# Kernel tuning notes

Hardware: AMD Instinct MI355X
Metric: run time of the kernel (lower is better)

Reference implementation:

```python
import jax, jax.numpy as jnp
import numpy as np

OUTCOMES = [8, 8, 8, 8, 8, 8]           # concept outcome counts (concepts_order)
N_TOTAL = int(np.prod(OUTCOMES))        # 262144 joint states
N_VALID = 8192                          # admissible states
B, D = 4096, 1024


def setup_inputs() -> dict:
    key = jax.random.key(0)
    k1, k2 = jax.random.split(key)
    embeddings = jax.random.normal(k1, (B, D), dtype=jnp.float32)
    W = jax.random.normal(k2, (N_VALID, D), dtype=jnp.float32) * 0.02
    b = jnp.zeros((N_VALID,), dtype=jnp.float32)
    # unique sorted admissible-state indices, like torch.argwhere(mask)
    rng = np.random.default_rng(0)
    valid_states = jnp.asarray(
        np.sort(rng.choice(N_TOTAL, size=N_VALID, replace=False)).astype(np.int32))
    return {"embeddings": embeddings, "W": W, "b": b, "valid_states": valid_states}


def reference(embeddings, W, b, valid_states):
    # softmax over valid states: [B, N_VALID]
    probs = jax.nn.softmax(embeddings @ W.T + b, axis=1)
    probs_t = probs.T  # [N_VALID, B] for leading-axis segment reduction
    marginals = []
    stride = N_TOTAL
    for n_i in OUTCOMES:
        stride //= n_i
        # digit of each valid joint-state index along this concept's axis
        digit = (valid_states // stride) % n_i  # [N_VALID]
        # equivalent to scattering probs into the full joint tensor and
        # summing over all other concept axes, without materializing it
        m = jax.ops.segment_sum(probs_t, digit, num_segments=n_i).T  # [B, n_i]
        marginals.append(m)
    return jnp.stack(marginals)  # [n_concepts, B, 8]
```

## Files before the change

kernel.cpp:

```cpp
#include <hip/hip_runtime.h>
#include <hip/hip_bf16.h>
#include <cstdint>
#include <cstddef>

typedef __bf16 bf16_t;
typedef bf16_t bf16x8 __attribute__((ext_vector_type(8)));
typedef bf16_t bf16x4 __attribute__((ext_vector_type(4)));
typedef float  f32x4  __attribute__((ext_vector_type(4)));
typedef unsigned int u32;

#define BROWS 4096
#define NV    8192
#define KD    1024
#define NT    16
#define ST    48
#define LOG2E 1.44269504088896340736f

#define GLL(gsrc, ldst) \
  __builtin_amdgcn_global_load_lds((const __attribute__((address_space(1))) u32*)(gsrc), \
                                   (__attribute__((address_space(3))) u32*)(ldst), 16, 0, 0)
#define FENCE asm volatile("" ::: "memory")

__global__ void cvt_kernel(const float* __restrict__ src, bf16_t* __restrict__ dst, int n4) {
  int idx = blockIdx.x * blockDim.x + threadIdx.x;
  int stride = gridDim.x * blockDim.x;
  for (int i = idx; i < n4; i += stride) {
    float4 v = ((const float4*)src)[i];
    bf16x4 o;
    o[0] = (bf16_t)v.x; o[1] = (bf16_t)v.y; o[2] = (bf16_t)v.z; o[3] = (bf16_t)v.w;
    ((bf16x4*)dst)[i] = o;
  }
}

__global__ void build_s2t_kernel(const int* __restrict__ vstate, bf16_t* __restrict__ s2t) {
  int g = blockIdx.x * blockDim.x + threadIdx.x;
  if (g >= ST * NV) return;
  int b = g >> 13;
  int ig = g & (NV - 1);
  int c = b >> 3;
  int d = b & 7;
  int src = ig ^ ((b & 7) << 3);
  int dig = (vstate[src] >> (15 - 3 * c)) & 7;
  s2t[g] = (bf16_t)(dig == d ? 1.0f : 0.0f);
}

__global__ __launch_bounds__(512, 2)
void gemm_fused_kernel(const bf16_t* __restrict__ W, const bf16_t* __restrict__ E,
                       const float* __restrict__ bias, const bf16_t* __restrict__ s2t,
                       float* __restrict__ part) {
  __shared__ __align__(16) char lds[2][65536];
  #define AKH0 0
  #define AKH1 16384
  #define BKH0 32768
  #define BKH1 49152

  const int t    = threadIdx.x;
  const int lane = t & 63;
  const int wv   = t >> 6;
  const int wm   = wv >> 2;
  const int wn   = wv & 3;
  const int fr   = lane & 15;
  const int fq   = lane >> 4;

  int bid = blockIdx.x;
  int wg  = (bid & 7) * 64 + (bid >> 3);
  const int stile = wg >> 4;
  const int btile = wg & 15;
  const int st0 = stile * 256;
  const int bt0 = btile * 256;

  const int srow = lane >> 2;
  const int skel = ((lane & 3) ^ ((lane >> 3) & 3)) * 8;
  const bf16_t* aptr = W + (size_t)(st0 + wv * 32 + srow) * KD + skel;
  const bf16_t* bptr = E + (size_t)(bt0 + wv * 32 + srow) * KD + skel;
  const int dchunk = (wv * 2) * 1024;

  const int xsw = (fr & 6) << 3;
  const int base_a = (((wm * 128 + fr) * 64 + fq * 16) ^ xsw);
  const int base_b = 32768 + (((wn * 64 + fr) * 64 + fq * 16) ^ xsw);

  f32x4 acc[8][4] = {};

  GLL(aptr, &lds[0][AKH0 + dchunk]);
  GLL(aptr + 16 * KD, &lds[0][AKH0 + dchunk + 1024]);
  GLL(bptr, &lds[0][BKH0 + dchunk]);
  GLL(bptr + 16 * KD, &lds[0][BKH0 + dchunk + 1024]);
  GLL(aptr + 32, &lds[0][AKH1 + dchunk]);
  GLL(aptr + 32 + 16 * KD, &lds[0][AKH1 + dchunk + 1024]);
  GLL(bptr + 32, &lds[0][BKH1 + dchunk]);
  GLL(bptr + 32 + 16 * KD, &lds[0][BKH1 + dchunk + 1024]);
  asm volatile("s_waitcnt vmcnt(0)" ::: "memory");
  __builtin_amdgcn_s_barrier();
  FENCE;

  int cur = 0;
  for (int kt = 0; kt < NT; ++kt) {
    const char* bufp = lds[cur];
    char* nbuf = lds[cur ^ 1];
    const bool pf = (kt + 1 < NT);

    bf16x8 a0[8], b0[4], a1[8], b1[4];

#pragma unroll
    for (int n = 0; n < 4; ++n)
      b0[n] = *(const bf16x8*)(bufp + base_b + n * 1024);
#pragma unroll
    for (int m = 0; m < 8; ++m)
      a0[m] = *(const bf16x8*)(bufp + base_a + m * 1024);

    if (pf) {
      const bf16_t* an = aptr + (kt + 1) * 64;
      const bf16_t* bn = bptr + (kt + 1) * 64;
      GLL(an, &nbuf[AKH0 + dchunk]);
      GLL(an + 16 * KD, &nbuf[AKH0 + dchunk + 1024]);
      GLL(bn, &nbuf[BKH0 + dchunk]);
      GLL(bn + 16 * KD, &nbuf[BKH0 + dchunk + 1024]);
      GLL(an + 32, &nbuf[AKH1 + dchunk]);
      GLL(an + 32 + 16 * KD, &nbuf[AKH1 + dchunk + 1024]);
      GLL(bn + 32, &nbuf[BKH1 + dchunk]);
      GLL(bn + 32 + 16 * KD, &nbuf[BKH1 + dchunk + 1024]);
    }

#pragma unroll
    for (int n = 0; n < 4; ++n)
      b1[n] = *(const bf16x8*)(bufp + base_b + 16384 + n * 1024);
#pragma unroll
    for (int m = 0; m < 8; ++m)
      a1[m] = *(const bf16x8*)(bufp + base_a + 16384 + m * 1024);

    __builtin_amdgcn_s_setprio(1);
#pragma unroll
    for (int m = 0; m < 8; ++m)
#pragma unroll
      for (int n = 0; n < 4; ++n)
        acc[m][n] = __builtin_amdgcn_mfma_f32_16x16x32_bf16(a0[m], b0[n], acc[m][n], 0, 0, 0);
#pragma unroll
    for (int m = 0; m < 8; ++m)
#pragma unroll
      for (int n = 0; n < 4; ++n)
        acc[m][n] = __builtin_amdgcn_mfma_f32_16x16x32_bf16(a1[m], b1[n], acc[m][n], 0, 0, 0);
    __builtin_amdgcn_s_setprio(0);

    asm volatile("s_waitcnt vmcnt(0)" ::: "memory");
    __builtin_amdgcn_sched_barrier(0);
    __builtin_amdgcn_s_barrier();
    FENCE;
    cur ^= 1;
  }

  char* const ldsf = &lds[0][0];
  {
#pragma unroll
    for (int q = 0; q < 3; ++q) {
      const bf16_t* src = s2t + (size_t)(wv * 6 + q * 2 + (lane >> 5)) * NV
                          + st0 + (lane & 31) * 8;
      GLL(src, ldsf + 65536 + wv * 3072 + q * 1024);
    }
  }

  float* const ppart = part + ((size_t)stile * BROWS + bt0) * ST;

#pragma unroll
  for (int pass = 0; pass < 2; ++pass) {
    if ((wn >> 1) == pass) {
#pragma unroll
      for (int m = 0; m < 8; ++m) {
        const float4 bb = *(const float4*)&bias[st0 + wm * 128 + m * 16 + fq * 4];
#pragma unroll
        for (int n = 0; n < 4; ++n) {
          bf16x4 ev;
          ev[0] = (bf16_t)exp2f((acc[m][n][0] + bb.x) * LOG2E);
          ev[1] = (bf16_t)exp2f((acc[m][n][1] + bb.y) * LOG2E);
          ev[2] = (bf16_t)exp2f((acc[m][n][2] + bb.z) * LOG2E);
          ev[3] = (bf16_t)exp2f((acc[m][n][3] + bb.w) * LOG2E);
          const int jh = (wn & 1) * 64 + n * 16 + fr;
          const int ib = (wm * 128 + m * 16 + fq * 4) * 2;
          *(bf16x4*)(ldsf + jh * 512 + (ib ^ ((fr & 7) << 4))) = ev;
        }
      }
    }
    if (pass == 0) asm volatile("s_waitcnt vmcnt(0)" ::: "memory");
    __syncthreads();

    f32x4 acc2[3] = {{0.f,0.f,0.f,0.f},{0.f,0.f,0.f,0.f},{0.f,0.f,0.f,0.f}};
#pragma unroll
    for (int k2 = 0; k2 < 8; ++k2) {
      const int ko = (k2 * 64 + fq * 16) ^ ((fr & 7) << 4);
      const bf16x8 ea = *(const bf16x8*)(ldsf + (wv * 16 + fr) * 512 + ko);
#pragma unroll
      for (int n2 = 0; n2 < 3; ++n2) {
        const bf16x8 sb = *(const bf16x8*)(ldsf + 65536 + (n2 * 16 + fr) * 512 + ko);
        acc2[n2] = __builtin_amdgcn_mfma_f32_16x16x32_bf16(ea, sb, acc2[n2], 0, 0, 0);
      }
    }
    const int jg = pass * 128 + wv * 16 + fq * 4;
#pragma unroll
    for (int n2 = 0; n2 < 3; ++n2)
#pragma unroll
      for (int r = 0; r < 4; ++r)
        ppart[(size_t)(jg + r) * ST + n2 * 16 + fr] = acc2[n2][r];
    __syncthreads();
  }
}

__global__ __launch_bounds__(64)
void reduce_kernel(const float* __restrict__ part, float* __restrict__ out) {
  const int b = blockIdx.x;
  const int t = threadIdx.x;
  __shared__ float fin[ST];
  if (t < ST) {
    float s = 0.f;
#pragma unroll
    for (int mt = 0; mt < 32; ++mt)
      s += part[((size_t)mt * BROWS + b) * ST + t];
    fin[t] = s;
  }
  __syncthreads();
  if (t < ST) {
    float total = fin[0] + fin[1] + fin[2] + fin[3] + fin[4] + fin[5] + fin[6] + fin[7];
    out[(size_t)(t >> 3) * BROWS * 8 + (size_t)b * 8 + (t & 7)] = fin[t] / total;
  }
}

extern "C" void kernel_launch(void* const* d_in, const int* in_sizes, int n_in,
                              void* d_out, int out_size, void* d_ws, size_t ws_size,
                              hipStream_t stream) {
  const float* E    = (const float*)d_in[0];
  const float* W    = (const float*)d_in[1];
  const float* bias = (const float*)d_in[2];
  const int*   vs   = (const int*)d_in[3];
  float* out = (float*)d_out;

  char* ws = (char*)d_ws;
  size_t off = 0;
  bf16_t* Eb   = (bf16_t*)(ws + off); off += (size_t)BROWS * KD * 2;
  bf16_t* Wb   = (bf16_t*)(ws + off); off += (size_t)NV * KD * 2;
  bf16_t* s2t  = (bf16_t*)(ws + off); off += (size_t)ST * NV * 2;
  float*  part = (float*)(ws + off);  off += (size_t)32 * BROWS * ST * 4;

  build_s2t_kernel<<<(ST * NV + 255) / 256, 256, 0, stream>>>(vs, s2t);
  cvt_kernel<<<2048, 256, 0, stream>>>(E, Eb, BROWS * KD / 4);
  cvt_kernel<<<2048, 256, 0, stream>>>(W, Wb, NV * KD / 4);
  gemm_fused_kernel<<<512, 512, 0, stream>>>(Wb, Eb, bias, s2t, part);
  reduce_kernel<<<BROWS, 64, 0, stream>>>(part, out);
}
```

Baseline: 106.2 us.

## Split GEMM k-tile into four barrier-phased stages with interleaved async loads

Restructures the main GEMM loop into four phases per k-tile. Each phase loads a quarter of the A fragments into registers, issues one slice of the next tile's global-to-LDS prefetch, and runs 16 MFMAs, with barriers between phases in a ping-pong style schedule. Waits become partial (vmcnt(4)) instead of draining all loads, so prefetch stays in flight across phases. Fewer live A registers lowers register pressure. The cost is many more workgroup barriers per iteration, and the partial vmcnt counting must stay exactly right for correctness. The epilogue's s2t staging offset is moved to fit the new flat LDS layout.

```diff
diff --git a/kernel.cpp b/kernel.cpp
--- a/kernel.cpp
+++ b/kernel.cpp
@@ -48,11 +48,7 @@
 void gemm_fused_kernel(const bf16_t* __restrict__ W, const bf16_t* __restrict__ E,
                        const float* __restrict__ bias, const bf16_t* __restrict__ s2t,
                        float* __restrict__ part) {
-  __shared__ __align__(16) char lds[2][65536];
-  #define AKH0 0
-  #define AKH1 16384
-  #define BKH0 32768
-  #define BKH1 49152
+  __shared__ __align__(16) char lds[131072];
 
   const int t    = threadIdx.x;
   const int lane = t & 63;
@@ -75,86 +71,129 @@
   const bf16_t* bptr = E + (size_t)(bt0 + wv * 32 + srow) * KD + skel;
   const int dchunk = (wv * 2) * 1024;
 
-  const int xsw = (fr & 6) << 3;
-  const int base_a = (((wm * 128 + fr) * 64 + fq * 16) ^ xsw);
-  const int base_b = 32768 + (((wn * 64 + fr) * 64 + fq * 16) ^ xsw);
+  const int xsw    = (fr & 6) << 3;
+  const int a_base = wm * 8192 + ((fr * 64 + fq * 16) ^ xsw);
+  const int b_base = wn * 4096 + ((fr * 64 + fq * 16) ^ xsw);
 
   f32x4 acc[8][4] = {};
 
-  GLL(aptr, &lds[0][AKH0 + dchunk]);
-  GLL(aptr + 16 * KD, &lds[0][AKH0 + dchunk + 1024]);
-  GLL(bptr, &lds[0][BKH0 + dchunk]);
-  GLL(bptr + 16 * KD, &lds[0][BKH0 + dchunk + 1024]);
-  GLL(aptr + 32, &lds[0][AKH1 + dchunk]);
-  GLL(aptr + 32 + 16 * KD, &lds[0][AKH1 + dchunk + 1024]);
-  GLL(bptr + 32, &lds[0][BKH1 + dchunk]);
-  GLL(bptr + 32 + 16 * KD, &lds[0][BKH1 + dchunk + 1024]);
-  asm volatile("s_waitcnt vmcnt(0)" ::: "memory");
+  GLL(aptr,                &lds[0 * 16384 + dchunk]);
+  GLL(aptr + 16 * KD,      &lds[0 * 16384 + dchunk + 1024]);
+  GLL(bptr,                &lds[1 * 16384 + dchunk]);
+  GLL(bptr + 16 * KD,      &lds[1 * 16384 + dchunk + 1024]);
+  GLL(aptr + 32,           &lds[2 * 16384 + dchunk]);
+  GLL(aptr + 32 + 16 * KD, &lds[2 * 16384 + dchunk + 1024]);
+  GLL(bptr + 32,           &lds[3 * 16384 + dchunk]);
+  GLL(bptr + 32 + 16 * KD, &lds[3 * 16384 + dchunk + 1024]);
+  asm volatile("s_waitcnt vmcnt(4)" ::: "memory");
   __builtin_amdgcn_s_barrier();
   FENCE;
 
-  int cur = 0;
   for (int kt = 0; kt < NT; ++kt) {
-    const char* bufp = lds[cur];
-    char* nbuf = lds[cur ^ 1];
+    const int cb = (kt & 1) * 4;
+    const int nb = ((kt + 1) & 1) * 4;
+    const char* sA0 = &lds[(cb + 0) * 16384];
+    const char* sB0 = &lds[(cb + 1) * 16384];
+    const char* sA1 = &lds[(cb + 2) * 16384];
+    const char* sB1 = &lds[(cb + 3) * 16384];
     const bool pf = (kt + 1 < NT);
-
-    bf16x8 a0[8], b0[4], a1[8], b1[4];
+    const int ko = (kt + 1) * 64;
+
+    bf16x8 a[4], b0[4], b1[4];
 
 #pragma unroll
     for (int n = 0; n < 4; ++n)
-      b0[n] = *(const bf16x8*)(bufp + base_b + n * 1024);
-#pragma unroll
-    for (int m = 0; m < 8; ++m)
-      a0[m] = *(const bf16x8*)(bufp + base_a + m * 1024);
-
-    if (pf) {
-      const bf16_t* an = aptr + (kt + 1) * 64;
-      const bf16_t* bn = bptr + (kt + 1) * 64;
-      GLL(an, &nbuf[AKH0 + dchunk]);
-      GLL(an + 16 * KD, &nbuf[AKH0 + dchunk + 1024]);
-      GLL(bn, &nbuf[BKH0 + dchunk]);
-      GLL(bn + 16 * KD, &nbuf[BKH0 + dchunk + 1024]);
-      GLL(an + 32, &nbuf[AKH1 + dchunk]);
-      GLL(an + 32 + 16 * KD, &nbuf[AKH1 + dchunk + 1024]);
-      GLL(bn + 32, &nbuf[BKH1 + dchunk]);
-      GLL(bn + 32 + 16 * KD, &nbuf[BKH1 + dchunk + 1024]);
-    }
+      b0[n] = *(const bf16x8*)(sB0 + b_base + n * 1024);
+#pragma unroll
+    for (int mi = 0; mi < 4; ++mi)
+      a[mi] = *(const bf16x8*)(sA0 + a_base + mi * 1024);
+    if (pf) {
+      GLL(aptr + ko,           &lds[(nb + 0) * 16384 + dchunk]);
+      GLL(aptr + ko + 16 * KD, &lds[(nb + 0) * 16384 + dchunk + 1024]);
+    }
+    FENCE; __builtin_amdgcn_s_barrier();
+    asm volatile("s_waitcnt lgkmcnt(0)" ::: "memory");
+    __builtin_amdgcn_sched_barrier(0);
+    __builtin_amdgcn_s_setprio(1);
+#pragma unroll
+    for (int mi = 0; mi < 4; ++mi)
+#pragma unroll
+      for (int n = 0; n < 4; ++n)
+        acc[mi][n] = __builtin_amdgcn_mfma_f32_16x16x32_bf16(a[mi], b0[n], acc[mi][n], 0, 0, 0);
+    __builtin_amdgcn_s_setprio(0);
+    FENCE; __builtin_amdgcn_s_barrier(); FENCE;
+
+#pragma unroll
+    for (int mi = 0; mi < 4; ++mi)
+      a[mi] = *(const bf16x8*)(sA0 + a_base + (4 + mi) * 1024);
+    if (pf) {
+      GLL(bptr + ko,           &lds[(nb + 1) * 16384 + dchunk]);
+      GLL(bptr + ko + 16 * KD, &lds[(nb + 1) * 16384 + dchunk + 1024]);
+    }
+    FENCE; __builtin_amdgcn_s_barrier();
+    asm volatile("s_waitcnt lgkmcnt(0)" ::: "memory");
+    __builtin_amdgcn_sched_barrier(0);
+    __builtin_amdgcn_s_setprio(1);
+#pragma unroll
+    for (int mi = 0; mi < 4; ++mi)
+#pragma unroll
+      for (int n = 0; n < 4; ++n)
+        acc[4 + mi][n] = __builtin_amdgcn_mfma_f32_16x16x32_bf16(a[mi], b0[n], acc[4 + mi][n], 0, 0, 0);
+    __builtin_amdgcn_s_setprio(0);
+    if (pf) asm volatile("s_waitcnt vmcnt(4)" ::: "memory");
+    else    asm volatile("s_waitcnt vmcnt(0)" ::: "memory");
+    FENCE; __builtin_amdgcn_s_barrier(); FENCE;
 
 #pragma unroll
     for (int n = 0; n < 4; ++n)
-      b1[n] = *(const bf16x8*)(bufp + base_b + 16384 + n * 1024);
-#pragma unroll
-    for (int m = 0; m < 8; ++m)
-      a1[m] = *(const bf16x8*)(bufp + base_a + 16384 + m * 1024);
-
-    __builtin_amdgcn_s_setprio(1);
-#pragma unroll
-    for (int m = 0; m < 8; ++m)
-#pragma unroll
-      for (int n = 0; n < 4; ++n)
-        acc[m][n] = __builtin_amdgcn_mfma_f32_16x16x32_bf16(a0[m], b0[n], acc[m][n], 0, 0, 0);
-#pragma unroll
-    for (int m = 0; m < 8; ++m)
-#pragma unroll
-      for (int n = 0; n < 4; ++n)
-        acc[m][n] = __builtin_amdgcn_mfma_f32_16x16x32_bf16(a1[m], b1[n], acc[m][n], 0, 0, 0);
-    __builtin_amdgcn_s_setprio(0);
-
-    asm volatile("s_waitcnt vmcnt(0)" ::: "memory");
-    __builtin_amdgcn_sched_barrier(0);
-    __builtin_amdgcn_s_barrier();
-    FENCE;
-    cur ^= 1;
-  }
-
-  char* const ldsf = &lds[0][0];
+      b1[n] = *(const bf16x8*)(sB1 + b_base + n * 1024);
+#pragma unroll
+    for (int mi = 0; mi < 4; ++mi)
+      a[mi] = *(const bf16x8*)(sA1 + a_base + mi * 1024);
+    if (pf) {
+      GLL(aptr + ko + 32,           &lds[(nb + 2) * 16384 + dchunk]);
+      GLL(aptr + ko + 32 + 16 * KD, &lds[(nb + 2) * 16384 + dchunk + 1024]);
+    }
+    FENCE; __builtin_amdgcn_s_barrier();
+    asm volatile("s_waitcnt lgkmcnt(0)" ::: "memory");
+    __builtin_amdgcn_sched_barrier(0);
+    __builtin_amdgcn_s_setprio(1);
+#pragma unroll
+    for (int mi = 0; mi < 4; ++mi)
+#pragma unroll
+      for (int n = 0; n < 4; ++n)
+        acc[mi][n] = __builtin_amdgcn_mfma_f32_16x16x32_bf16(a[mi], b1[n], acc[mi][n], 0, 0, 0);
+    __builtin_amdgcn_s_setprio(0);
+    FENCE; __builtin_amdgcn_s_barrier(); FENCE;
+
+#pragma unroll
+    for (int mi = 0; mi < 4; ++mi)
+      a[mi] = *(const bf16x8*)(sA1 + a_base + (4 + mi) * 1024);
+    if (pf) {
+      GLL(bptr + ko + 32,           &lds[(nb + 3) * 16384 + dchunk]);
+      GLL(bptr + ko + 32 + 16 * KD, &lds[(nb + 3) * 16384 + dchunk + 1024]);
+    }
+    FENCE; __builtin_amdgcn_s_barrier();
+    asm volatile("s_waitcnt lgkmcnt(0)" ::: "memory");
+    __builtin_amdgcn_sched_barrier(0);
+    __builtin_amdgcn_s_setprio(1);
+#pragma unroll
+    for (int mi = 0; mi < 4; ++mi)
+#pragma unroll
+      for (int n = 0; n < 4; ++n)
+        acc[4 + mi][n] = __builtin_amdgcn_mfma_f32_16x16x32_bf16(a[mi], b1[n], acc[4 + mi][n], 0, 0, 0);
+    __builtin_amdgcn_s_setprio(0);
+    if (pf) asm volatile("s_waitcnt vmcnt(4)" ::: "memory");
+    FENCE; __builtin_amdgcn_s_barrier(); FENCE;
+  }
+
+  char* const ldsf = &lds[0];
   {
 #pragma unroll
     for (int q = 0; q < 3; ++q) {
       const bf16_t* src = s2t + (size_t)(wv * 6 + q * 2 + (lane >> 5)) * NV
                           + st0 + (lane & 31) * 8;
-      GLL(src, ldsf + 65536 + wv * 3072 + q * 1024);
+      GLL(src, ldsf + 98304 + wv * 3072 + q * 1024);
     }
   }
 
@@ -185,11 +224,11 @@
     f32x4 acc2[3] = {{0.f,0.f,0.f,0.f},{0.f,0.f,0.f,0.f},{0.f,0.f,0.f,0.f}};
 #pragma unroll
     for (int k2 = 0; k2 < 8; ++k2) {
-      const int ko = (k2 * 64 + fq * 16) ^ ((fr & 7) << 4);
-      const bf16x8 ea = *(const bf16x8*)(ldsf + (wv * 16 + fr) * 512 + ko);
+      const int ko2 = (k2 * 64 + fq * 16) ^ ((fr & 7) << 4);
+      const bf16x8 ea = *(const bf16x8*)(ldsf + (wv * 16 + fr) * 512 + ko2);
 #pragma unroll
       for (int n2 = 0; n2 < 3; ++n2) {
-        const bf16x8 sb = *(const bf16x8*)(ldsf + 65536 + (n2 * 16 + fr) * 512 + ko);
+        const bf16x8 sb = *(const bf16x8*)(ldsf + 98304 + (n2 * 16 + fr) * 512 + ko2);
         acc2[n2] = __builtin_amdgcn_mfma_f32_16x16x32_bf16(ea, sb, acc2[n2], 0, 0, 0);
       }
     }
```

Result: slower. 109.3 us (+3.0%).
